# Kernel optimization log

Measured on AMD Instinct MI355X. Metric: run time of the kernel, lower is better.

## Reference

```python
import jax, jax.numpy as jnp
import numpy as np

N = 4096          # total nodes (num_source + num_target)
S = 2048          # num_source
D = 128           # node feature dim
NUM_ADJ = 2       # len(adj)
NUM_LAYERS = 2    # GIN propagation layers
DENSITY = 0.002   # adjacency density (~8 neighbors/node)
RAW_LS = 4.993284 # inverse-softplus(5.0): model.covar_module.lengthscale = 5.0


def setup_inputs() -> dict:
    key = jax.random.key(0)
    k1, k2 = jax.random.split(key)
    feat = jax.random.normal(k1, (N, D), jnp.float32)
    adj = (jax.random.uniform(k2, (NUM_ADJ, N, N)) < DENSITY).astype(jnp.float32)
    return {
        "feat": feat,
        "adj": adj,
        "raw_lengthscale": jnp.full((1, 1), RAW_LS, jnp.float32),
        "raw_varsigma_w": jnp.zeros((1, 1), jnp.float32),
        "raw_sigma_w": jnp.zeros((1, 1), jnp.float32),
        "raw_sigma_b": jnp.zeros((1, 1), jnp.float32),
        "raw_s_alpha": jnp.zeros((NUM_ADJ, 1), jnp.float32),
        "raw_t_alpha": jnp.zeros((NUM_ADJ, 1), jnp.float32),
        "x1": jnp.arange(N, dtype=jnp.int32),
        "x2": jnp.arange(N, dtype=jnp.int32),
    }


def _graphgp_cov(feat, adj, raw_lengthscale, raw_varsigma_w, raw_sigma_w,
                 raw_sigma_b, raw_s_alpha, raw_t_alpha):
    sp = jax.nn.softplus  # gpytorch Positive() constraint transform
    ls = sp(raw_lengthscale)[0, 0]
    vw = sp(raw_varsigma_w)[0, 0]
    sw = sp(raw_sigma_w)[0, 0]
    sb = sp(raw_sigma_b)[0, 0]
    s_alpha = sp(raw_s_alpha)[:, 0]
    t_alpha = sp(raw_t_alpha)[:, 0]

    # RBF base covariance on all node features: exp(-||xi-xj||^2 / (2 ls^2))
    x = feat / ls
    sq_norm = jnp.sum(x * x, axis=1)
    sq = jnp.maximum(sq_norm[:, None] + sq_norm[None, :] - 2.0 * (x @ x.T), 0.0)
    C0 = jnp.exp(-0.5 * sq)

    src = jnp.arange(N) < S
    block_mask = (src[:, None] == src[None, :]).astype(feat.dtype)
    adj_b = adj * block_mask  # block-diagonal restriction (only i == j branch survives)

    def adj_conv(K):
        out = jnp.zeros_like(K)
        for i in range(NUM_ADJ):
            A = adj_b[i]
            temp = A @ (A @ K).T  # A K^T A^T
            out = out + (sb ** 2 + sw ** 2 * temp) * (s_alpha[i] * t_alpha[i])
        return out

    def relu_cov(K):
        s = jnp.sqrt(jnp.diag(K))[:, None] + 1e-5
        c = jnp.clip(K / (s * s.T), -1.0 + 1e-6, 1.0 - 1e-6)
        theta = jnp.arccos(c)
        return (0.5 / np.pi) * (jnp.sin(theta) + (np.pi - theta) * jnp.cos(theta)) * (s * s.T)

    K = vw ** 2 * adj_conv(C0)
    for _ in range(NUM_LAYERS - 1):
        K = vw ** 2 * adj_conv(relu_cov(K))

    # block-mean reweighting (index_K)
    m_ss = K[:S, :S].mean()
    m_tt = K[S:, S:].mean()
    m_st = K[:S, S:].mean()
    ss = src[:, None] & src[None, :]
    tt = (~src)[:, None] & (~src)[None, :]
    index_K = jnp.where(ss, m_ss, jnp.where(tt, m_tt, m_st))
    return K * index_K


def reference(feat, adj, raw_lengthscale, raw_varsigma_w, raw_sigma_w,
              raw_sigma_b, raw_s_alpha, raw_t_alpha, x1, x2):
    K = _graphgp_cov(feat, adj, raw_lengthscale, raw_varsigma_w, raw_sigma_w,
                     raw_sigma_b, raw_s_alpha, raw_t_alpha)
    return K[x1[:, None], x2[None, :]]
```

## Files before the change

### kernel.cpp

```cpp
#include <hip/hip_runtime.h>
#include <math.h>

#define NN 4096
#define SS 2048
#define DD 128
#define NADJ 2
#define MAXNNZ 64
#define HB 2048

typedef short v8s __attribute__((ext_vector_type(8)));
typedef float v4f __attribute__((ext_vector_type(4)));

__device__ __forceinline__ float softplusf(float x) {
    if (x > 20.f) return x;
    if (x < -20.f) return expf(x);
    return log1pf(expf(x));
}

__device__ __forceinline__ ushort f2bf(float f) {
    unsigned int u = __float_as_uint(f);
    unsigned int r = (u + 0x7fff + ((u >> 16) & 1)) >> 16;
    return (ushort)r;
}
__device__ __forceinline__ float bf2f(ushort h) {
    return __uint_as_float(((unsigned int)h) << 16);
}
__device__ __forceinline__ float blo(unsigned int u) { return __uint_as_float(u << 16); }
__device__ __forceinline__ float bhi(unsigned int u) { return __uint_as_float(u & 0xffff0000u); }

__global__ void params_kernel(const float* rls, const float* rvw, const float* rsw,
                              const float* rsb, const float* rsa, const float* rta,
                              float* params, double* sums) {
    if (threadIdx.x == 0) {
        float ls = softplusf(rls[0]);
        float vw = softplusf(rvw[0]);
        float sw = softplusf(rsw[0]);
        float sb = softplusf(rsb[0]);
        float a0 = softplusf(rsa[0]) * softplusf(rta[0]);
        float a1 = softplusf(rsa[1]) * softplusf(rta[1]);
        float vw2 = vw * vw, sw2 = sw * sw, sb2 = sb * sb;
        params[0] = 1.f / ls;
        params[1] = vw2 * sb2 * (a0 + a1);
        params[2] = vw2 * sw2 * a0;
        params[3] = vw2 * sw2 * a1;
        sums[0] = 0.0; sums[1] = 0.0; sums[2] = 0.0;
    }
}

__global__ void xb_kernel(const float* feat, const float* params, ushort* xb, float* xn) {
    int r = blockIdx.x;
    int l = threadIdx.x;
    float inv_ls = params[0];
    ushort h0 = f2bf(feat[r * DD + l] * inv_ls);
    ushort h1 = f2bf(feat[r * DD + 64 + l] * inv_ls);
    xb[r * DD + l] = h0;
    xb[r * DD + 64 + l] = h1;
    float v0 = bf2f(h0), v1 = bf2f(h1);
    float s = v0 * v0 + v1 * v1;
    for (int off = 32; off; off >>= 1) s += __shfl_xor(s, off);
    if (l == 0) xn[r] = s;
}

__global__ __launch_bounds__(256) void c0_mfma_kernel(const ushort* xb, const float* xn,
                                                      ushort* C0b) {
    __shared__ float xr[128], xc[128];
    int t = threadIdx.x;
    int r0 = blockIdx.y * 128, c0 = blockIdx.x * 128;
    if (t < 128) xr[t] = xn[r0 + t];
    else xc[t - 128] = xn[c0 + (t - 128)];
    __syncthreads();

    int w = t >> 6, l = t & 63;
    int wr = w >> 1, wc = w & 1;
    int lr = l & 15;
    int lk = (l >> 4) * 8;
    const ushort* pa = xb + (size_t)(r0 + wr * 64 + lr) * DD + lk;
    const ushort* pb = xb + (size_t)(c0 + wc * 64 + lr) * DD + lk;

    v4f acc[4][4] = {};
    for (int ks = 0; ks < 4; ks++) {
        v8s a[4], b[4];
        for (int m = 0; m < 4; m++) a[m] = *(const v8s*)(pa + (size_t)m * 16 * DD + ks * 32);
        for (int n = 0; n < 4; n++) b[n] = *(const v8s*)(pb + (size_t)n * 16 * DD + ks * 32);
        for (int m = 0; m < 4; m++)
            for (int n = 0; n < 4; n++)
                acc[m][n] = __builtin_amdgcn_mfma_f32_16x16x32_bf16(a[m], b[n], acc[m][n], 0, 0, 0);
    }

    int rbase = wr * 64;
    int cbase = wc * 64;
    for (int m = 0; m < 4; m++) {
        for (int n = 0; n < 4; n++) {
            int ocol = cbase + n * 16 + lr;
            float xnc = xc[ocol];
            for (int j = 0; j < 4; j++) {
                int orow = rbase + m * 16 + (l >> 4) * 4 + j;
                float sq = xr[orow] + xnc - 2.f * acc[m][n][j];
                sq = fmaxf(sq, 0.f);
                C0b[(size_t)(r0 + orow) * NN + c0 + ocol] = f2bf(expf(-0.5f * sq));
            }
        }
    }
}

__global__ void extract_kernel(const float* adj, int* nnzc, int* colsa) {
    __shared__ int sc[MAXNNZ];
    int b = blockIdx.x;
    int i = b >> 12;
    int r = b & (NN - 1);
    int lane = threadIdx.x;
    int base = (r < SS) ? 0 : SS;
    const float* arow = adj + ((size_t)i * NN + r) * NN + base;
    int cnt = 0;
    for (int it = 0; it < SS / 64; ++it) {
        int c = it * 64 + lane;
        float v = arow[c];
        unsigned long long m = __ballot(v != 0.f);
        if (v != 0.f) {
            int pos = cnt + __popcll(m & ((1ull << lane) - 1ull));
            if (pos < MAXNNZ) sc[pos] = c;
        }
        cnt += __popcll(m);
    }
    if (cnt > MAXNNZ) cnt = MAXNNZ;
    __syncthreads();
    if (lane < cnt) colsa[(size_t)b * MAXNNZ + lane] = base + sc[lane];
    if (lane == 0) nnzc[b] = cnt;
}

__global__ void merge_kernel(const int* nnzc, const int* colsa, ushort* moff, ushort* colinfo) {
    int c = blockIdx.x * 256 + threadIdx.x;
    if (c >= NN) return;
    int base = (c < SS) ? 0 : SS;
    int n0 = nnzc[c], n1 = nnzc[NN + c];
    int c0 = n0 < 8 ? n0 : 8;
    int c1 = n1 < 8 ? n1 : 8;
    ushort e[16];
    #pragma unroll
    for (int i = 0; i < 16; i++) e[i] = 8192;
    for (int i = 0; i < c0; i++)
        e[i] = (ushort)((colsa[(size_t)c * MAXNNZ + i] - base) * 4);
    for (int i = 0; i < c1; i++)
        e[c0 + i] = (ushort)((2056 + colsa[(size_t)(NN + c) * MAXNNZ + i] - base) * 4);
    uint4* mo = (uint4*)(moff + (size_t)c * 16);
    mo[0] = *(uint4*)&e[0];
    mo[1] = *(uint4*)&e[8];
    colinfo[c] = (ushort)((n0 > 8 || n1 > 8) ? 1 : 0);
}

__global__ void diag1_kernel(const ushort* C0b, const int* nnzc, const int* colsa,
                             const float* params, float* svec) {
    int t = threadIdx.x;
    int r = blockIdx.x * 4 + (t >> 6);
    int lane = t & 63;
    float c_add = params[1], w0 = params[2], w1 = params[3];
    float s = 0.f;
    for (int a = 0; a < 2; a++) {
        int b = a * NN + r;
        int cnt = nnzc[b];
        const int* crow = colsa + (size_t)b * MAXNNZ;
        int myk = crow[(lane < cnt) ? lane : 0];
        float wa = a ? w1 : w0;
        float acc = 0.f;
        for (int j = 0; j < cnt; j++) {
            int row = crow[j];
            if (lane < cnt) acc += bf2f(C0b[(size_t)row * NN + myk]);
        }
        s += wa * acc;
    }
    for (int off = 32; off; off >>= 1) s += __shfl_xor(s, off);
    if (lane == 0) {
        float d = c_add + s;
        svec[r] = sqrtf(fmaxf(d, 0.f)) + 1e-5f;
    }
}

template <int MODE>
__global__ __launch_bounds__(256, 4) void conv_kernel(const ushort* __restrict__ Kb,
                                                      const int* __restrict__ nnzc,
                                                      const int* __restrict__ colsa,
                                                      const uint4* __restrict__ moffq,
                                                      const ushort* __restrict__ colinfo,
                                                      const float* __restrict__ params,
                                                      const float* __restrict__ svec,
                                                      void* __restrict__ Kout_,
                                                      double* __restrict__ sums) {
    __shared__ float rs[4112];
    __shared__ double red[256];
    int zone = blockIdx.x;
    int by = blockIdx.y;
    int r = (zone == 2) ? SS + by : by;
    int h = (zone >= 1) ? 1 : 0;
    int cstart = (zone == 1) ? 0 : by;
    int cbase = h * HB;
    int t = threadIdx.x;
    float c_add = params[1], w0 = params[2], w1 = params[3];

    {
        int cnt0 = nnzc[r], cnt1 = nnzc[NN + r];
        const int* crow0 = colsa + (size_t)r * MAXNNZ;
        const int* crow1 = colsa + (size_t)(NN + r) * MAXNNZ;
        int4 ia0 = *(const int4*)crow0;
        int4 ib0 = *(const int4*)(crow0 + 4);
        int4 ia1 = *(const int4*)crow1;
        int4 ib1 = *(const int4*)(crow1 + 4);
        int id0[8] = {ia0.x, ia0.y, ia0.z, ia0.w, ib0.x, ib0.y, ib0.z, ib0.w};
        int id1[8] = {ia1.x, ia1.y, ia1.z, ia1.w, ib1.x, ib1.y, ib1.z, ib1.w};

        uint4 v0[8], v1[8];
        #pragma unroll
        for (int j = 0; j < 8; j++) {
            int row0 = (j < cnt0) ? id0[j] : 0;
            int row1 = (j < cnt1) ? id1[j] : 0;
            v0[j] = *(const uint4*)(Kb + (size_t)row0 * NN + cbase + t * 8);
            v1[j] = *(const uint4*)(Kb + (size_t)row1 * NN + cbase + t * 8);
        }

        float acc0[8], acc1[8];
        #pragma unroll
        for (int e = 0; e < 8; e++) { acc0[e] = 0.f; acc1[e] = 0.f; }
        #pragma unroll
        for (int j = 0; j < 8; j++) {
            if (j < cnt0) {
                uint4 v = v0[j];
                acc0[0] += blo(v.x); acc0[1] += bhi(v.x);
                acc0[2] += blo(v.y); acc0[3] += bhi(v.y);
                acc0[4] += blo(v.z); acc0[5] += bhi(v.z);
                acc0[6] += blo(v.w); acc0[7] += bhi(v.w);
            }
            if (j < cnt1) {
                uint4 v = v1[j];
                acc1[0] += blo(v.x); acc1[1] += bhi(v.x);
                acc1[2] += blo(v.y); acc1[3] += bhi(v.y);
                acc1[4] += blo(v.z); acc1[5] += bhi(v.z);
                acc1[6] += blo(v.w); acc1[7] += bhi(v.w);
            }
        }
        for (int j = 8; j < cnt0; j++) {
            uint4 v = *(const uint4*)(Kb + (size_t)crow0[j] * NN + cbase + t * 8);
            acc0[0] += blo(v.x); acc0[1] += bhi(v.x);
            acc0[2] += blo(v.y); acc0[3] += bhi(v.y);
            acc0[4] += blo(v.z); acc0[5] += bhi(v.z);
            acc0[6] += blo(v.w); acc0[7] += bhi(v.w);
        }
        for (int j = 8; j < cnt1; j++) {
            uint4 v = *(const uint4*)(Kb + (size_t)crow1[j] * NN + cbase + t * 8);
            acc1[0] += blo(v.x); acc1[1] += bhi(v.x);
            acc1[2] += blo(v.y); acc1[3] += bhi(v.y);
            acc1[4] += blo(v.z); acc1[5] += bhi(v.z);
            acc1[6] += blo(v.w); acc1[7] += bhi(v.w);
        }
        *(float4*)&rs[8 * t]            = {acc0[0]*w0, acc0[1]*w0, acc0[2]*w0, acc0[3]*w0};
        *(float4*)&rs[8 * t + 4]        = {acc0[4]*w0, acc0[5]*w0, acc0[6]*w0, acc0[7]*w0};
        *(float4*)&rs[2056 + 8 * t]     = {acc1[0]*w1, acc1[1]*w1, acc1[2]*w1, acc1[3]*w1};
        *(float4*)&rs[2056 + 8 * t + 4] = {acc1[4]*w1, acc1[5]*w1, acc1[6]*w1, acc1[7]*w1};
        if (t < 8) { rs[2048 + t] = 0.f; rs[4104 + t] = 0.f; }
    }
    __syncthreads();

    float sr = (MODE == 0) ? svec[r] : 0.f;
    double dsum = 0.0;
    ushort* out_b = (ushort*)Kout_;
    float* out_f = (float*)Kout_;
    const char* rsb = (const char*)rs;
    int n_u = (HB - cstart + 255) >> 8;

    #pragma unroll
    for (int mb = 0; mb < 2; mb++) {
        if (mb * 4 >= n_u) break;
        int cols[4];
        uint4 mo[4][2];
        ushort ci[4];
        #pragma unroll
        for (int q = 0; q < 4; q++) {
            int u = mb * 4 + q;
            int c_rel = cstart + t + 256 * u;
            bool act = (u < n_u) && (c_rel < HB);
            int col = cbase + (act ? c_rel : 0);
            const uint4* mop = moffq + (size_t)col * 2;
            mo[q][0] = mop[0];
            mo[q][1] = mop[1];
            ci[q] = colinfo[col];
            cols[q] = act ? col : -1;
        }
        float ac[4];
        #pragma unroll
        for (int q = 0; q < 4; q++) {
            uint4 m0 = mo[q][0], m1 = mo[q][1];
            float s0 = *(const float*)(rsb + (m0.x & 0xffffu))
                     + *(const float*)(rsb + (m0.x >> 16));
            float s1 = *(const float*)(rsb + (m0.y & 0xffffu))
                     + *(const float*)(rsb + (m0.y >> 16));
            float s2 = *(const float*)(rsb + (m0.z & 0xffffu))
                     + *(const float*)(rsb + (m0.z >> 16));
            float s3 = *(const float*)(rsb + (m0.w & 0xffffu))
                     + *(const float*)(rsb + (m0.w >> 16));
            float s4 = *(const float*)(rsb + (m1.x & 0xffffu))
                     + *(const float*)(rsb + (m1.x >> 16));
            float s5 = *(const float*)(rsb + (m1.y & 0xffffu))
                     + *(const float*)(rsb + (m1.y >> 16));
            float s6 = *(const float*)(rsb + (m1.z & 0xffffu))
                     + *(const float*)(rsb + (m1.z >> 16));
            float s7 = *(const float*)(rsb + (m1.w & 0xffffu))
                     + *(const float*)(rsb + (m1.w >> 16));
            ac[q] = ((s0 + s1) + (s2 + s3)) + ((s4 + s5) + (s6 + s7));
        }
        #pragma unroll
        for (int q = 0; q < 4; q++) {
            int col = cols[q];
            if (col < 0) continue;
            float acc = ac[q];
            if (ci[q] & 1) {
                for (int a = 0; a < 2; a++) {
                    int b = a * NN + col;
                    int cnt = nnzc[b];
                    if (cnt > 8) {
                        const int* cp = colsa + (size_t)b * MAXNNZ;
                        for (int k = 8; k < cnt; k++)
                            acc += rs[(cp[k] & (HB - 1)) + (a ? 2056 : 0)];
                    }
                }
            }
            float kv = c_add + acc;
            if (MODE == 0) {
                const float PIF = 3.14159265358979323846f;
                const float INV2PI = 0.15915494309189535f;
                float pp = sr * svec[col];
                float cc = kv / pp;
                cc = fminf(fmaxf(cc, -1.f + 1e-6f), 1.f - 1e-6f);
                float th = acosf(cc);
                float sth = sqrtf(fmaxf(1.f - cc * cc, 0.f));
                kv = INV2PI * (sth + (PIF - th) * cc) * pp;
                out_b[(size_t)r * NN + col] = f2bf(kv);
            } else {
                out_f[(size_t)r * NN + col] = kv;
                int c_rel = col - cbase;
                if (zone == 1) dsum += (double)kv;
                else dsum += (c_rel == by) ? (double)kv : 2.0 * (double)kv;
            }
        }
    }

    if (MODE == 1) {
        red[t] = dsum;
        __syncthreads();
        for (int off = 128; off; off >>= 1) {
            if (t < off) red[t] += red[t + off];
            __syncthreads();
        }
        if (t == 0) atomicAdd(&sums[zone], red[0]);
    }
}

__global__ __launch_bounds__(256) void mirror_kernel(ushort* Kb) {
    int bi = blockIdx.x;
    int bj = blockIdx.y;
    if (bj < bi) return;
    __shared__ ushort lds[64][66];
    int R0 = bi * 64, C0 = bj * 64;
    int t = threadIdx.x;
    #pragma unroll
    for (int k = 0; k < 16; k++) {
        int lin = k * 256 + t;
        int row = lin >> 6, col = lin & 63;
        lds[row][col] = Kb[(size_t)(R0 + row) * NN + C0 + col];
    }
    __syncthreads();
    if (bj > bi) {
        #pragma unroll
        for (int k = 0; k < 16; k++) {
            int lin = k * 256 + t;
            int row = lin >> 6, col = lin & 63;
            Kb[(size_t)(C0 + row) * NN + R0 + col] = lds[col][row];
        }
    } else {
        #pragma unroll
        for (int k = 0; k < 16; k++) {
            int lin = k * 256 + t;
            int row = lin >> 6, col = lin & 63;
            if (row > col) Kb[(size_t)(R0 + row) * NN + R0 + col] = lds[col][row];
        }
    }
}

__global__ __launch_bounds__(256) void finalize_kernel(float* out, const double* sums) {
    int bi = blockIdx.x;
    int bj = blockIdx.y;
    if (bj < bi) return;
    __shared__ float lds[64][65];
    const double inv = 1.0 / (2048.0 * 2048.0);
    float mss = (float)(sums[0] * inv);
    float mst = (float)(sums[1] * inv);
    float mtt = (float)(sums[2] * inv);
    int R0 = bi * 64, C0 = bj * 64;
    float m = (R0 < SS) ? (C0 < SS ? mss : mst) : (C0 < SS ? mst : mtt);
    int t = threadIdx.x;
    #pragma unroll
    for (int k = 0; k < 16; k++) {
        int lin = k * 256 + t;
        int row = lin >> 6, col = lin & 63;
        lds[row][col] = out[(size_t)(R0 + row) * NN + C0 + col];
    }
    __syncthreads();
    if (bj > bi) {
        #pragma unroll
        for (int k = 0; k < 16; k++) {
            int lin = k * 256 + t;
            int row = lin >> 6, col = lin & 63;
            out[(size_t)(R0 + row) * NN + C0 + col] = m * lds[row][col];
            out[(size_t)(C0 + row) * NN + R0 + col] = m * lds[col][row];
        }
    } else {
        #pragma unroll
        for (int k = 0; k < 16; k++) {
            int lin = k * 256 + t;
            int row = lin >> 6, col = lin & 63;
            float v = (row <= col) ? lds[row][col] : lds[col][row];
            out[(size_t)(R0 + row) * NN + R0 + col] = m * v;
        }
    }
}

extern "C" void kernel_launch(void* const* d_in, const int* in_sizes, int n_in,
                              void* d_out, int out_size, void* d_ws, size_t ws_size,
                              hipStream_t stream) {
    const float* feat = (const float*)d_in[0];
    const float* adj  = (const float*)d_in[1];
    const float* rls  = (const float*)d_in[2];
    const float* rvw  = (const float*)d_in[3];
    const float* rsw  = (const float*)d_in[4];
    const float* rsb  = (const float*)d_in[5];
    const float* rsa  = (const float*)d_in[6];
    const float* rta  = (const float*)d_in[7];
    float* out = (float*)d_out;

    const size_t PNN = (size_t)NN * NN;
    char* p = (char*)d_ws;
    auto alloc = [&](size_t bytes) {
        char* r = p;
        p += (bytes + 255) & ~(size_t)255;
        return r;
    };
    float*  params   = (float*)alloc(64);
    double* sums     = (double*)alloc(64);
    float*  xn       = (float*)alloc((size_t)NN * 4);
    float*  svec     = (float*)alloc((size_t)NN * 4);
    int*    nnzc     = (int*)alloc((size_t)2 * NN * 4);
    int*    colsa    = (int*)alloc((size_t)2 * NN * MAXNNZ * 4);
    ushort* moff     = (ushort*)alloc((size_t)NN * 16 * 2);
    ushort* colinfo  = (ushort*)alloc((size_t)NN * 2);
    ushort* xb       = (ushort*)alloc((size_t)NN * DD * 2);
    ushort* cb0      = (ushort*)alloc(PNN * 2);
    ushort* kb1      = (ushort*)alloc(PNN * 2);

    params_kernel<<<1, 64, 0, stream>>>(rls, rvw, rsw, rsb, rsa, rta, params, sums);
    xb_kernel<<<NN, 64, 0, stream>>>(feat, params, xb, xn);
    c0_mfma_kernel<<<dim3(NN / 128, NN / 128), 256, 0, stream>>>(xb, xn, cb0);
    extract_kernel<<<NADJ * NN, 64, 0, stream>>>(adj, nnzc, colsa);
    merge_kernel<<<(NN + 255) / 256, 256, 0, stream>>>(nnzc, colsa, moff, colinfo);

    diag1_kernel<<<NN / 4, 256, 0, stream>>>(cb0, nnzc, colsa, params, svec);

    conv_kernel<0><<<dim3(3, HB), 256, 0, stream>>>(cb0, nnzc, colsa, (const uint4*)moff,
                                                    colinfo, params, svec, kb1, sums);
    mirror_kernel<<<dim3(64, 64), 256, 0, stream>>>(kb1);

    conv_kernel<1><<<dim3(3, HB), 256, 0, stream>>>(kb1, nnzc, colsa, (const uint4*)moff,
                                                    colinfo, params, svec, out, sums);

    finalize_kernel<<<dim3(64, 64), 256, 0, stream>>>(out, sums);
}
```

Measured before the change: 264.8 us.

## Precompute block means algebraically and fold reweighting into second conv pass

Block means of the final covariance are computed ahead of time from column-count weighted sums of the mirrored first-layer matrix (sum of A K A^T = sum over K weighted by adjacency column counts), so the second conv pass writes already-scaled outputs. The finalize step shrinks to a pure lower-triangle mirror with no rescale read-modify-write of the upper half. The conv kernel also processes two rows per block, sharing the column offset loads and the LDS gather indices between them. The cost is an extra pass over the bf16 matrix plus atomic-based count kernels, and double the shared memory per block.

New measurement: 350.8 us. +32.5%, slower.

```diff
diff --git a/kernel.cpp b/kernel.cpp
--- a/kernel.cpp
+++ b/kernel.cpp
@@ -148,6 +148,15 @@
     colinfo[c] = (ushort)((n0 > 8 || n1 > 8) ? 1 : 0);
 }
 
+__global__ void colcnt_kernel(const int* nnzc, const int* colsa, int* colcnt) {
+    int b = blockIdx.x * 256 + threadIdx.x;
+    if (b >= 2 * NN) return;
+    int cnt = nnzc[b];
+    const int* crow = colsa + (size_t)b * MAXNNZ;
+    int abase = (b >> 12) << 12;
+    for (int k = 0; k < cnt; k++) atomicAdd(&colcnt[abase + crow[k]], 1);
+}
+
 __global__ void diag1_kernel(const ushort* C0b, const int* nnzc, const int* colsa,
                              const float* params, float* svec) {
     int t = threadIdx.x;
@@ -175,6 +184,53 @@
     }
 }
 
+__global__ __launch_bounds__(256) void msum_kernel(const ushort* __restrict__ Kb,
+                                                   const int* __restrict__ colcnt,
+                                                   const float* __restrict__ params,
+                                                   double* sums) {
+    __shared__ double rlo[256], rhi[256];
+    int j = blockIdx.x;
+    int t = threadIdx.x;
+    float w0 = params[2], w1 = params[3];
+    float wj0 = w0 * (float)colcnt[j];
+    float wj1 = w1 * (float)colcnt[NN + j];
+    const ushort* row = Kb + (size_t)j * NN + t * 16;
+    const int* cc0 = colcnt + t * 16;
+    const int* cc1 = colcnt + NN + t * 16;
+    float s = 0.f;
+    #pragma unroll
+    for (int e = 0; e < 16; e++) {
+        float kv = bf2f(row[e]);
+        s += kv * (wj0 * (float)cc0[e] + wj1 * (float)cc1[e]);
+    }
+    bool lo = (t < 128);
+    rlo[t] = lo ? (double)s : 0.0;
+    rhi[t] = lo ? 0.0 : (double)s;
+    __syncthreads();
+    for (int off = 128; off; off >>= 1) {
+        if (t < off) { rlo[t] += rlo[t + off]; rhi[t] += rhi[t + off]; }
+        __syncthreads();
+    }
+    if (t == 0) {
+        if (j < SS) {
+            atomicAdd(&sums[0], rlo[0]);
+            atomicAdd(&sums[1], rhi[0]);
+        } else {
+            atomicAdd(&sums[2], rhi[0]);
+        }
+    }
+}
+
+__global__ void means_kernel(const float* params, const double* sums, float* meansbuf) {
+    if (threadIdx.x == 0) {
+        const double inv = 1.0 / (2048.0 * 2048.0);
+        double c_add = (double)params[1];
+        meansbuf[0] = (float)(c_add + sums[0] * inv);
+        meansbuf[1] = (float)(c_add + sums[1] * inv);
+        meansbuf[2] = (float)(c_add + sums[2] * inv);
+    }
+}
+
 template <int MODE>
 __global__ __launch_bounds__(256, 4) void conv_kernel(const ushort* __restrict__ Kb,
                                                       const int* __restrict__ nnzc,
@@ -183,20 +239,20 @@
                                                       const ushort* __restrict__ colinfo,
                                                       const float* __restrict__ params,
                                                       const float* __restrict__ svec,
-                                                      void* __restrict__ Kout_,
-                                                      double* __restrict__ sums) {
-    __shared__ float rs[4112];
-    __shared__ double red[256];
+                                                      const float* __restrict__ meansbuf,
+                                                      void* __restrict__ Kout_) {
+    __shared__ float rs[2][4112];
     int zone = blockIdx.x;
     int by = blockIdx.y;
-    int r = (zone == 2) ? SS + by : by;
+    int r0 = (zone == 2) ? SS + 2 * by : 2 * by;
     int h = (zone >= 1) ? 1 : 0;
-    int cstart = (zone == 1) ? 0 : by;
+    int cstart = (zone == 1) ? 0 : 2 * by;
     int cbase = h * HB;
     int t = threadIdx.x;
     float c_add = params[1], w0 = params[2], w1 = params[3];
 
-    {
+    for (int g = 0; g < 2; g++) {
+        int r = r0 + g;
         int cnt0 = nnzc[r], cnt1 = nnzc[NN + r];
         const int* crow0 = colsa + (size_t)r * MAXNNZ;
         const int* crow1 = colsa + (size_t)(NN + r) * MAXNNZ;
@@ -250,19 +306,21 @@
             acc1[4] += blo(v.z); acc1[5] += bhi(v.z);
             acc1[6] += blo(v.w); acc1[7] += bhi(v.w);
         }
-        *(float4*)&rs[8 * t]            = {acc0[0]*w0, acc0[1]*w0, acc0[2]*w0, acc0[3]*w0};
-        *(float4*)&rs[8 * t + 4]        = {acc0[4]*w0, acc0[5]*w0, acc0[6]*w0, acc0[7]*w0};
-        *(float4*)&rs[2056 + 8 * t]     = {acc1[0]*w1, acc1[1]*w1, acc1[2]*w1, acc1[3]*w1};
-        *(float4*)&rs[2056 + 8 * t + 4] = {acc1[4]*w1, acc1[5]*w1, acc1[6]*w1, acc1[7]*w1};
-        if (t < 8) { rs[2048 + t] = 0.f; rs[4104 + t] = 0.f; }
+        *(float4*)&rs[g][8 * t]            = {acc0[0]*w0, acc0[1]*w0, acc0[2]*w0, acc0[3]*w0};
+        *(float4*)&rs[g][8 * t + 4]        = {acc0[4]*w0, acc0[5]*w0, acc0[6]*w0, acc0[7]*w0};
+        *(float4*)&rs[g][2056 + 8 * t]     = {acc1[0]*w1, acc1[1]*w1, acc1[2]*w1, acc1[3]*w1};
+        *(float4*)&rs[g][2056 + 8 * t + 4] = {acc1[4]*w1, acc1[5]*w1, acc1[6]*w1, acc1[7]*w1};
+        if (t < 8) { rs[g][2048 + t] = 0.f; rs[g][4104 + t] = 0.f; }
     }
     __syncthreads();
 
-    float sr = (MODE == 0) ? svec[r] : 0.f;
-    double dsum = 0.0;
+    float sr0 = 0.f, sr1 = 0.f, m = 0.f;
+    if (MODE == 0) { sr0 = svec[r0]; sr1 = svec[r0 + 1]; }
+    else m = meansbuf[zone];
     ushort* out_b = (ushort*)Kout_;
     float* out_f = (float*)Kout_;
-    const char* rsb = (const char*)rs;
+    const char* rsbA = (const char*)&rs[0][0];
+    const char* rsbB = (const char*)&rs[1][0];
     int n_u = (HB - cstart + 255) >> 8;
 
     #pragma unroll
@@ -283,72 +341,75 @@
             ci[q] = colinfo[col];
             cols[q] = act ? col : -1;
         }
-        float ac[4];
+        float acA[4], acB[4];
         #pragma unroll
         for (int q = 0; q < 4; q++) {
             uint4 m0 = mo[q][0], m1 = mo[q][1];
-            float s0 = *(const float*)(rsb + (m0.x & 0xffffu))
-                     + *(const float*)(rsb + (m0.x >> 16));
-            float s1 = *(const float*)(rsb + (m0.y & 0xffffu))
-                     + *(const float*)(rsb + (m0.y >> 16));
-            float s2 = *(const float*)(rsb + (m0.z & 0xffffu))
-                     + *(const float*)(rsb + (m0.z >> 16));
-            float s3 = *(const float*)(rsb + (m0.w & 0xffffu))
-                     + *(const float*)(rsb + (m0.w >> 16));
-            float s4 = *(const float*)(rsb + (m1.x & 0xffffu))
-                     + *(const float*)(rsb + (m1.x >> 16));
-            float s5 = *(const float*)(rsb + (m1.y & 0xffffu))
-                     + *(const float*)(rsb + (m1.y >> 16));
-            float s6 = *(const float*)(rsb + (m1.z & 0xffffu))
-                     + *(const float*)(rsb + (m1.z >> 16));
-            float s7 = *(const float*)(rsb + (m1.w & 0xffffu))
-                     + *(const float*)(rsb + (m1.w >> 16));
-            ac[q] = ((s0 + s1) + (s2 + s3)) + ((s4 + s5) + (s6 + s7));
+            uint o0 = m0.x & 0xffffu, o1 = m0.x >> 16;
+            uint o2 = m0.y & 0xffffu, o3 = m0.y >> 16;
+            uint o4 = m0.z & 0xffffu, o5 = m0.z >> 16;
+            uint o6 = m0.w & 0xffffu, o7 = m0.w >> 16;
+            uint o8 = m1.x & 0xffffu, o9 = m1.x >> 16;
+            uint oA = m1.y & 0xffffu, oB = m1.y >> 16;
+            uint oC = m1.z & 0xffffu, oD = m1.z >> 16;
+            uint oE = m1.w & 0xffffu, oF = m1.w >> 16;
+            float a0 = *(const float*)(rsbA + o0) + *(const float*)(rsbA + o1);
+            float b0 = *(const float*)(rsbB + o0) + *(const float*)(rsbB + o1);
+            float a1 = *(const float*)(rsbA + o2) + *(const float*)(rsbA + o3);
+            float b1 = *(const float*)(rsbB + o2) + *(const float*)(rsbB + o3);
+            float a2 = *(const float*)(rsbA + o4) + *(const float*)(rsbA + o5);
+            float b2 = *(const float*)(rsbB + o4) + *(const float*)(rsbB + o5);
+            float a3 = *(const float*)(rsbA + o6) + *(const float*)(rsbA + o7);
+            float b3 = *(const float*)(rsbB + o6) + *(const float*)(rsbB + o7);
+            float a4 = *(const float*)(rsbA + o8) + *(const float*)(rsbA + o9);
+            float b4 = *(const float*)(rsbB + o8) + *(const float*)(rsbB + o9);
+            float a5 = *(const float*)(rsbA + oA) + *(const float*)(rsbA + oB);
+            float b5 = *(const float*)(rsbB + oA) + *(const float*)(rsbB + oB);
+            float a6 = *(const float*)(rsbA + oC) + *(const float*)(rsbA + oD);
+            float b6 = *(const float*)(rsbB + oC) + *(const float*)(rsbB + oD);
+            float a7 = *(const float*)(rsbA + oE) + *(const float*)(rsbA + oF);
+            float b7 = *(const float*)(rsbB + oE) + *(const float*)(rsbB + oF);
+            acA[q] = ((a0 + a1) + (a2 + a3)) + ((a4 + a5) + (a6 + a7));
+            acB[q] = ((b0 + b1) + (b2 + b3)) + ((b4 + b5) + (b6 + b7));
         }
         #pragma unroll
         for (int q = 0; q < 4; q++) {
             int col = cols[q];
             if (col < 0) continue;
-            float acc = ac[q];
+            float accA = acA[q], accB = acB[q];
             if (ci[q] & 1) {
                 for (int a = 0; a < 2; a++) {
                     int b = a * NN + col;
                     int cnt = nnzc[b];
                     if (cnt > 8) {
                         const int* cp = colsa + (size_t)b * MAXNNZ;
-                        for (int k = 8; k < cnt; k++)
-                            acc += rs[(cp[k] & (HB - 1)) + (a ? 2056 : 0)];
+                        for (int k = 8; k < cnt; k++) {
+                            int idx = (cp[k] & (HB - 1)) + (a ? 2056 : 0);
+                            accA += rs[0][idx];
+                            accB += rs[1][idx];
+                        }
                     }
                 }
             }
-            float kv = c_add + acc;
+            float kvA = c_add + accA;
+            float kvB = c_add + accB;
             if (MODE == 0) {
                 const float PIF = 3.14159265358979323846f;
                 const float INV2PI = 0.15915494309189535f;
-                float pp = sr * svec[col];
-                float cc = kv / pp;
-                cc = fminf(fmaxf(cc, -1.f + 1e-6f), 1.f - 1e-6f);
-                float th = acosf(cc);
-                float sth = sqrtf(fmaxf(1.f - cc * cc, 0.f));
-                kv = INV2PI * (sth + (PIF - th) * cc) * pp;
-                out_b[(size_t)r * NN + col] = f2bf(kv);
+                float sc = svec[col];
+                float pA = sr0 * sc, pB = sr1 * sc;
+                float cA = fminf(fmaxf(kvA / pA, -1.f + 1e-6f), 1.f - 1e-6f);
+                float cB = fminf(fmaxf(kvB / pB, -1.f + 1e-6f), 1.f - 1e-6f);
+                float thA = acosf(cA), thB = acosf(cB);
+                float stA = sqrtf(fmaxf(1.f - cA * cA, 0.f));
+                float stB = sqrtf(fmaxf(1.f - cB * cB, 0.f));
+                out_b[(size_t)r0 * NN + col] = f2bf(INV2PI * (stA + (PIF - thA) * cA) * pA);
+                out_b[(size_t)(r0 + 1) * NN + col] = f2bf(INV2PI * (stB + (PIF - thB) * cB) * pB);
             } else {
-                out_f[(size_t)r * NN + col] = kv;
-                int c_rel = col - cbase;
-                if (zone == 1) dsum += (double)kv;
-                else dsum += (c_rel == by) ? (double)kv : 2.0 * (double)kv;
+                out_f[(size_t)r0 * NN + col] = kvA * m;
+                out_f[(size_t)(r0 + 1) * NN + col] = kvB * m;
             }
         }
-    }
-
-    if (MODE == 1) {
-        red[t] = dsum;
-        __syncthreads();
-        for (int off = 128; off; off >>= 1) {
-            if (t < off) red[t] += red[t + off];
-            __syncthreads();
-        }
-        if (t == 0) atomicAdd(&sums[zone], red[0]);
     }
 }
 
@@ -383,17 +444,12 @@
     }
 }
 
-__global__ __launch_bounds__(256) void finalize_kernel(float* out, const double* sums) {
+__global__ __launch_bounds__(256) void mirror_f32_kernel(float* out) {
     int bi = blockIdx.x;
     int bj = blockIdx.y;
     if (bj < bi) return;
     __shared__ float lds[64][65];
-    const double inv = 1.0 / (2048.0 * 2048.0);
-    float mss = (float)(sums[0] * inv);
-    float mst = (float)(sums[1] * inv);
-    float mtt = (float)(sums[2] * inv);
     int R0 = bi * 64, C0 = bj * 64;
-    float m = (R0 < SS) ? (C0 < SS ? mss : mst) : (C0 < SS ? mst : mtt);
     int t = threadIdx.x;
     #pragma unroll
     for (int k = 0; k < 16; k++) {
@@ -407,16 +463,14 @@
         for (int k = 0; k < 16; k++) {
             int lin = k * 256 + t;
             int row = lin >> 6, col = lin & 63;
-            out[(size_t)(R0 + row) * NN + C0 + col] = m * lds[row][col];
-            out[(size_t)(C0 + row) * NN + R0 + col] = m * lds[col][row];
+            out[(size_t)(C0 + row) * NN + R0 + col] = lds[col][row];
         }
     } else {
         #pragma unroll
         for (int k = 0; k < 16; k++) {
             int lin = k * 256 + t;
             int row = lin >> 6, col = lin & 63;
-            float v = (row <= col) ? lds[row][col] : lds[col][row];
-            out[(size_t)(R0 + row) * NN + R0 + col] = m * v;
+            if (row > col) out[(size_t)(R0 + row) * NN + R0 + col] = lds[col][row];
         }
     }
 }
@@ -443,30 +497,37 @@
     };
     float*  params   = (float*)alloc(64);
     double* sums     = (double*)alloc(64);
+    float*  meansbuf = (float*)alloc(64);
     float*  xn       = (float*)alloc((size_t)NN * 4);
     float*  svec     = (float*)alloc((size_t)NN * 4);
     int*    nnzc     = (int*)alloc((size_t)2 * NN * 4);
     int*    colsa    = (int*)alloc((size_t)2 * NN * MAXNNZ * 4);
     ushort* moff     = (ushort*)alloc((size_t)NN * 16 * 2);
     ushort* colinfo  = (ushort*)alloc((size_t)NN * 2);
+    int*    colcnt   = (int*)alloc((size_t)2 * NN * 4);
     ushort* xb       = (ushort*)alloc((size_t)NN * DD * 2);
     ushort* cb0      = (ushort*)alloc(PNN * 2);
     ushort* kb1      = (ushort*)alloc(PNN * 2);
 
     params_kernel<<<1, 64, 0, stream>>>(rls, rvw, rsw, rsb, rsa, rta, params, sums);
+    hipMemsetAsync(colcnt, 0, (size_t)2 * NN * 4, stream);
     xb_kernel<<<NN, 64, 0, stream>>>(feat, params, xb, xn);
     c0_mfma_kernel<<<dim3(NN / 128, NN / 128), 256, 0, stream>>>(xb, xn, cb0);
     extract_kernel<<<NADJ * NN, 64, 0, stream>>>(adj, nnzc, colsa);
     merge_kernel<<<(NN + 255) / 256, 256, 0, stream>>>(nnzc, colsa, moff, colinfo);
+    colcnt_kernel<<<(2 * NN + 255) / 256, 256, 0, stream>>>(nnzc, colsa, colcnt);
 
     diag1_kernel<<<NN / 4, 256, 0, stream>>>(cb0, nnzc, colsa, params, svec);
 
-    conv_kernel<0><<<dim3(3, HB), 256, 0, stream>>>(cb0, nnzc, colsa, (const uint4*)moff,
-                                                    colinfo, params, svec, kb1, sums);
+    conv_kernel<0><<<dim3(3, HB / 2), 256, 0, stream>>>(cb0, nnzc, colsa, (const uint4*)moff,
+                                                        colinfo, params, svec, meansbuf, kb1);
     mirror_kernel<<<dim3(64, 64), 256, 0, stream>>>(kb1);
 
-    conv_kernel<1><<<dim3(3, HB), 256, 0, stream>>>(kb1, nnzc, colsa, (const uint4*)moff,
-                                                    colinfo, params, svec, out, sums);
-
-    finalize_kernel<<<dim3(64, 64), 256, 0, stream>>>(out, sums);
-}
+    msum_kernel<<<NN, 256, 0, stream>>>(kb1, colcnt, params, sums);
+    means_kernel<<<1, 64, 0, stream>>>(params, sums, meansbuf);
+
+    conv_kernel<1><<<dim3(3, HB / 2), 256, 0, stream>>>(kb1, nnzc, colsa, (const uint4*)moff,
+                                                        colinfo, params, svec, meansbuf, out);
+
+    mirror_f32_kernel<<<dim3(64, 64), 256, 0, stream>>>(out);
+}
```
